# Kernel tuning notes

Measured on AMD Instinct MI355X. Metric: run time of the kernel, lower is better.

The kernel has to match this reference:

```python
import jax, jax.numpy as jnp
import numpy as np

CODEBOOK_SIZE = 1024
EMBED_DIM = 512
DECAY = 0.99
EPS = 1e-05


def setup_inputs() -> dict:
    key = jax.random.key(0)
    k1, k2, k3 = jax.random.split(key, 3)
    z = jax.random.normal(k1, (32, 2048, EMBED_DIM), dtype=jnp.float32)
    embedding = jax.random.normal(k2, (CODEBOOK_SIZE, EMBED_DIM), dtype=jnp.float32)
    cluster_size = jnp.ones((CODEBOOK_SIZE,), dtype=jnp.float32)
    embed_avg = jax.random.normal(k3, (CODEBOOK_SIZE, EMBED_DIM), dtype=jnp.float32)
    return {"z": z, "embedding": embedding, "cluster_size": cluster_size, "embed_avg": embed_avg}


def reference(z, embedding, cluster_size, embed_avg):
    # Flatten tokens: [N, D]
    z_flat = z.reshape(-1, EMBED_DIM)

    # Squared-L2 distances to codebook via expansion: ||z||^2 - 2 z.E^T + ||e||^2 -> [N, K]
    z_sq = jnp.sum(z_flat * z_flat, axis=1, keepdims=True)                 # [N, 1]
    e_sq = jnp.sum(embedding * embedding, axis=1)                          # [K]
    distances = z_sq - 2.0 * (z_flat @ embedding.T) + e_sq[None, :]        # [N, K]
    indices = jnp.argmin(distances, axis=1)                                # [N] int

    # Codebook gather (quantized vectors)
    quantized = embedding[indices].reshape(z.shape)

    # --- EMA codebook update (training-mode math, deterministic part) ---
    used_counts = jax.ops.segment_sum(
        jnp.ones_like(indices, dtype=z_flat.dtype), indices, num_segments=CODEBOOK_SIZE)
    embed_sum = jax.ops.segment_sum(
        jax.lax.stop_gradient(z_flat), indices, num_segments=CODEBOOK_SIZE)  # [K, D]

    new_cluster_size = DECAY * cluster_size + (1.0 - DECAY) * used_counts
    new_embed_avg = DECAY * embed_avg + (1.0 - DECAY) * embed_sum
    n = jnp.sum(new_cluster_size)
    smoothed = (new_cluster_size + EPS) / (n + CODEBOOK_SIZE * EPS) * n
    new_embedding = new_embed_avg / smoothed[:, None]

    # Straight-through estimator
    quantized_st = z + jax.lax.stop_gradient(quantized - z)

    return (quantized_st, indices.reshape(z.shape[:-1]),
            new_embedding, new_cluster_size, new_embed_avg)
```

## Files before the change

### kernel.cpp

```cpp
#include <hip/hip_runtime.h>
#include <cfloat>

#define NTOK 65536
#define DIM  512
#define KCB  1024
#define TAU  0.12f
#define REF_CAP 4096

typedef unsigned short u16;
typedef __attribute__((ext_vector_type(8))) _Float16 half8;
typedef __attribute__((ext_vector_type(4))) float f32x4;

#define AS1(p) ((const __attribute__((address_space(1))) void*)(p))
#define AS3(p) ((__attribute__((address_space(3))) void*)(p))


__device__ __forceinline__ u16 h2u(_Float16 h) {
    u16 u; __builtin_memcpy(&u, &h, 2); return u;
}

__global__ __launch_bounds__(256) void esq_kernel(const float* __restrict__ E,
                                                  float* __restrict__ esq)
{
    const int lane = threadIdx.x & 63;
    const int wv   = threadIdx.x >> 6;
    const int k    = blockIdx.x * 4 + wv;
    const float* er = E + (size_t)k * DIM + lane * 8;
    float4 a = *(const float4*)er;
    float4 b = *(const float4*)(er + 4);
    float s = a.x*a.x + a.y*a.y + a.z*a.z + a.w*a.w
            + b.x*b.x + b.y*b.y + b.z*b.z + b.w*b.w;
    for (int off = 32; off > 0; off >>= 1) s += __shfl_down(s, off, 64);
    if (lane == 0) esq[k] = s;
}

__global__ __launch_bounds__(256) void ehalf_kernel(const float* __restrict__ E,
                                                    u16* __restrict__ Ehf)
{
    const size_t i = (size_t)blockIdx.x * 256 + threadIdx.x;
    const float2 v = *(const float2*)(E + i * 2);
    const _Float16 h0 = (_Float16)v.x, h1 = (_Float16)v.y;
    ((unsigned int*)Ehf)[i] = ((unsigned int)h2u(h1) << 16) | h2u(h0);
}

#define CVT(ZH, ZL, J, VAL) { const _Float16 hv_ = (_Float16)(VAL); \
    (ZH)[J] = hv_; (ZL)[J] = (_Float16)((VAL) - (float)hv_); }

#define LOADK(KC, ZH, ZL) { \
    const float4 a_ = *(const float4*)(zr + (KC) * 32); \
    const float4 b_ = *(const float4*)(zr + (KC) * 32 + 4); \
    CVT(ZH, ZL, 0, a_.x) CVT(ZH, ZL, 1, a_.y) \
    CVT(ZH, ZL, 2, a_.z) CVT(ZH, ZL, 3, a_.w) \
    CVT(ZH, ZL, 4, b_.x) CVT(ZH, ZL, 5, b_.y) \
    CVT(ZH, ZL, 6, b_.z) CVT(ZH, ZL, 7, b_.w) }

#define DSOFF(KC) const int off##KC = lo16 * 512 + \
    (((((KC) << 2) | hi16) ^ lo16) << 3);

#define KSTEP(KC, ZH, ZL) { \
    const half8 eh_ = *(const half8*)&ehi_t[off##KC]; \
    accA = __builtin_amdgcn_mfma_f32_16x16x32_f16((ZH), eh_, accA, 0, 0, 0); \
    accB = __builtin_amdgcn_mfma_f32_16x16x32_f16((ZL), eh_, accB, 0, 0, 0); }

#define STAGE { \
    __builtin_amdgcn_global_load_lds(AS1(gp0), AS3(&ehi_t[c0 * 512]), 16, 0, 0); \
    __builtin_amdgcn_global_load_lds(AS1(gp1), AS3(&ehi_t[c1 * 512]), 16, 0, 0); \
    __builtin_amdgcn_global_load_lds(AS1(gp2), AS3(&ehi_t[c2 * 512]), 16, 0, 0); \
    __builtin_amdgcn_global_load_lds(AS1(gp3), AS3(&ehi_t[c3 * 512]), 16, 0, 0); \
    gp0 += 8192; gp1 += 8192; gp2 += 8192; gp3 += 8192; }

__global__ __launch_bounds__(256, 1) void score_kernel(
    const float* __restrict__ z,
    const u16* __restrict__ Ehf,
    const float* __restrict__ esq,
    int* __restrict__ idx_ws, float* __restrict__ idx_out,
    int* __restrict__ refCount, int* __restrict__ refList)
{
    __shared__ _Float16 ehi_t[16 * 512];
    __shared__ float esq_lds[KCB];

    const int tid  = threadIdx.x;
    const int lane = tid & 63;
    const int wv   = tid >> 6;
    const int lo16 = lane & 15;
    const int hi16 = lane >> 4;
    const int blk  = blockIdx.x;
    const int tokbase = blk * 64 + wv * 16;

    for (int i = tid; i < KCB; i += 256) esq_lds[i] = esq[i];

    const float* zr = z + (size_t)(tokbase + lo16) * DIM + (hi16 << 3);
    half8 zh0,zh1,zh2,zh3,zh4,zh5,zh6,zh7,zh8,zh9,zh10,zh11,zh12,zh13,zh14,zh15;
    half8 zl0,zl1,zl2,zl3,zl4,zl5,zl6,zl7,zl8,zl9,zl10,zl11,zl12,zl13,zl14,zl15;
    LOADK(0,  zh0,  zl0)  LOADK(1,  zh1,  zl1)  LOADK(2,  zh2,  zl2)
    LOADK(3,  zh3,  zl3)  LOADK(4,  zh4,  zl4)  LOADK(5,  zh5,  zl5)
    LOADK(6,  zh6,  zl6)  LOADK(7,  zh7,  zl7)  LOADK(8,  zh8,  zl8)
    LOADK(9,  zh9,  zl9)  LOADK(10, zh10, zl10) LOADK(11, zh11, zl11)
    LOADK(12, zh12, zl12) LOADK(13, zh13, zl13) LOADK(14, zh14, zl14)
    LOADK(15, zh15, zl15)

    DSOFF(0)  DSOFF(1)  DSOFF(2)  DSOFF(3)
    DSOFF(4)  DSOFF(5)  DSOFF(6)  DSOFF(7)
    DSOFF(8)  DSOFF(9)  DSOFF(10) DSOFF(11)
    DSOFF(12) DSOFF(13) DSOFF(14) DSOFF(15)

    const int c0 = (wv << 2), c1 = c0 + 1, c2 = c0 + 2, c3 = c0 + 3;
    const u16* gp0 = Ehf + (size_t)c0 * 512 + ((lane ^ c0) << 3);
    const u16* gp1 = Ehf + (size_t)c1 * 512 + ((lane ^ c1) << 3);
    const u16* gp2 = Ehf + (size_t)c2 * 512 + ((lane ^ c2) << 3);
    const u16* gp3 = Ehf + (size_t)c3 * 512 + ((lane ^ c3) << 3);

    float d1[4], d2[4]; int i1[4];
    #pragma unroll
    for (int r = 0; r < 4; ++r) { d1[r] = FLT_MAX; d2[r] = FLT_MAX; i1[r] = KCB; }

    for (int ch = 0; ch < 64; ++ch) {
        __syncthreads();
        STAGE
        __syncthreads();

        const float ej = esq_lds[(ch << 4) + lo16];
        f32x4 accA = {0.f, 0.f, 0.f, 0.f};
        f32x4 accB = {0.f, 0.f, 0.f, 0.f};
        KSTEP(0,  zh0,  zl0)  KSTEP(1,  zh1,  zl1)  KSTEP(2,  zh2,  zl2)
        KSTEP(3,  zh3,  zl3)  KSTEP(4,  zh4,  zl4)  KSTEP(5,  zh5,  zl5)
        KSTEP(6,  zh6,  zl6)  KSTEP(7,  zh7,  zl7)  KSTEP(8,  zh8,  zl8)
        KSTEP(9,  zh9,  zl9)  KSTEP(10, zh10, zl10) KSTEP(11, zh11, zl11)
        KSTEP(12, zh12, zl12) KSTEP(13, zh13, zl13) KSTEP(14, zh14, zl14)
        KSTEP(15, zh15, zl15)

        const int code = (ch << 4) + lo16;
        #pragma unroll
        for (int r = 0; r < 4; ++r) {
            const float dist = fmaf(-2.0f, accB[r], fmaf(-2.0f, accA[r], ej));
            if (dist < d1[r]) { d2[r] = d1[r]; d1[r] = dist; i1[r] = code; }
            else              { d2[r] = fminf(d2[r], dist); }
        }
    }

    #pragma unroll
    for (int off = 1; off < 16; off <<= 1) {
        #pragma unroll
        for (int r = 0; r < 4; ++r) {
            const float od1 = __shfl_xor(d1[r], off, 64);
            const int   oi1 = __shfl_xor(i1[r], off, 64);
            const float od2 = __shfl_xor(d2[r], off, 64);
            float loser;
            if (od1 < d1[r] || (od1 == d1[r] && oi1 < i1[r])) {
                loser = d1[r]; d1[r] = od1; i1[r] = oi1;
            } else {
                loser = od1;
            }
            d2[r] = fminf(fminf(d2[r], od2), loser);
        }
    }
    if (lo16 == 0) {
        #pragma unroll
        for (int r = 0; r < 4; ++r) {
            const int token = tokbase + (hi16 << 2) + r;
            idx_ws[token]  = i1[r];
            idx_out[token] = (float)i1[r];
            if (d2[r] - d1[r] < TAU) {
                int slot = atomicAdd(refCount, 1);
                if (slot < REF_CAP) refList[slot] = token;
            }
        }
    }
}

__global__ __launch_bounds__(256) void refine_kernel(
    const float* __restrict__ z, const float* __restrict__ E,
    const int* __restrict__ refCount, const int* __restrict__ refList,
    int* __restrict__ idx_ws, float* __restrict__ idx_out)
{
    __shared__ double dists[KCB];
    const int tid = threadIdx.x;
    const int grp = tid >> 4;
    const int q   = tid & 15;
    int rc = *refCount; if (rc > REF_CAP) rc = REF_CAP;
    for (int r = blockIdx.x; r < rc; r += gridDim.x) {
        const int token = refList[r];
        double zr[32];
        {
            const float* zp = z + (size_t)token * DIM + q * 32;
            #pragma unroll
            for (int j = 0; j < 8; ++j) {
                const float4 v = *(const float4*)(zp + j * 4);
                zr[j*4+0] = (double)v.x; zr[j*4+1] = (double)v.y;
                zr[j*4+2] = (double)v.z; zr[j*4+3] = (double)v.w;
            }
        }
        for (int c = grp; c < KCB; c += 32) {
            const int c2 = c + 16;
            const float* ep  = E + (size_t)c  * DIM + q * 32;
            const float* ep2 = E + (size_t)c2 * DIM + q * 32;
            double s = 0.0, s2 = 0.0;
            #pragma unroll
            for (int j = 0; j < 8; ++j) {
                const float4 a = *(const float4*)(ep  + j * 4);
                const float4 b = *(const float4*)(ep2 + j * 4);
                double d;
                d = zr[j*4+0] - (double)a.x; s  = fma(d, d, s);
                d = zr[j*4+1] - (double)a.y; s  = fma(d, d, s);
                d = zr[j*4+2] - (double)a.z; s  = fma(d, d, s);
                d = zr[j*4+3] - (double)a.w; s  = fma(d, d, s);
                d = zr[j*4+0] - (double)b.x; s2 = fma(d, d, s2);
                d = zr[j*4+1] - (double)b.y; s2 = fma(d, d, s2);
                d = zr[j*4+2] - (double)b.z; s2 = fma(d, d, s2);
                d = zr[j*4+3] - (double)b.w; s2 = fma(d, d, s2);
            }
            #pragma unroll
            for (int off = 1; off < 16; off <<= 1) {
                s  += __shfl_xor(s,  off, 64);
                s2 += __shfl_xor(s2, off, 64);
            }
            if (q == 0) { dists[c] = s; dists[c2] = s2; }
        }
        __syncthreads();
        if (tid < 64) {
            const int lane = tid;
            double best = dists[lane]; int bi = lane;
            for (int c = lane + 64; c < KCB; c += 64) {
                const double dv = dists[c];
                if (dv < best) { best = dv; bi = c; }
            }
            for (int off = 32; off > 0; off >>= 1) {
                const double ob = __shfl_down(best, off, 64);
                const int    oi = __shfl_down(bi, off, 64);
                if (ob < best || (ob == best && oi < bi)) { best = ob; bi = oi; }
            }
            if (lane == 0) { idx_ws[token] = bi; idx_out[token] = (float)bi; }
        }
        __syncthreads();
    }
}

__global__ __launch_bounds__(256) void hist_kernel(const int* __restrict__ idx,
                                                   int* __restrict__ counts)
{
    __shared__ int h[KCB];
    const int tid = threadIdx.x;
    for (int i = tid; i < KCB; i += 256) h[i] = 0;
    __syncthreads();
    const int b0 = blockIdx.x * 1024;
    #pragma unroll
    for (int j = 0; j < 4; ++j) atomicAdd(&h[idx[b0 + j * 256 + tid]], 1);
    __syncthreads();
    for (int i = tid; i < KCB; i += 256) {
        const int v = h[i];
        if (v) atomicAdd(&counts[i], v);
    }
}

__global__ __launch_bounds__(1024) void scan_kernel(const int* __restrict__ counts,
                                                    int* __restrict__ cursor,
                                                    int* __restrict__ base)
{
    const int tid = threadIdx.x, lane = tid & 63, wv = tid >> 6;
    const int v = counts[tid];
    int s = v;
    #pragma unroll
    for (int off = 1; off < 64; off <<= 1) {
        const int nb = __shfl_up(s, off, 64);
        if (lane >= off) s += nb;
    }
    __shared__ int wsum[16], wbase[16];
    if (lane == 63) wsum[wv] = s;
    __syncthreads();
    if (tid == 0) {
        int r = 0;
        for (int w = 0; w < 16; ++w) { wbase[w] = r; r += wsum[w]; }
    }
    __syncthreads();
    const int excl = wbase[wv] + s - v;
    cursor[tid] = excl;
    base[tid]   = excl;
}

__global__ __launch_bounds__(256) void scatter_kernel(const int* __restrict__ idx,
                                                      int* __restrict__ cursor,
                                                      int* __restrict__ toklist)
{
    const int b0 = blockIdx.x * 1024;
    #pragma unroll
    for (int j = 0; j < 4; ++j) {
        const int t = b0 + j * 256 + threadIdx.x;
        const int k = idx[t];
        const int slot = atomicAdd(&cursor[k], 1);
        toklist[slot] = t;
    }
}

__global__ __launch_bounds__(256) void seg_sum_kernel(
    const float* __restrict__ z, const float* __restrict__ E,
    const int* __restrict__ toklist, const int* __restrict__ idx,
    float* __restrict__ out0, float* __restrict__ esum)
{
    __shared__ int toks[64];
    __shared__ int ks[64];
    const int tid  = threadIdx.x;
    const int seg0 = blockIdx.x * 64;
    if (tid < 64) toks[tid] = toklist[seg0 + tid];
    __syncthreads();
    if (tid < 64) ks[tid] = idx[toks[tid]];
    __syncthreads();

    const int d = tid * 2;
    int curk = ks[0];
    float2 er  = *(const float2*)(E + (size_t)curk * DIM + d);
    float2 acc = {0.f, 0.f};
    float2 v   = *(const float2*)(z + (size_t)toks[0] * DIM + d);
    for (int i = 0; i < 64; ++i) {
        const int t = toks[i];
        float2 vn;
        if (i < 63) vn = *(const float2*)(z + (size_t)toks[i + 1] * DIM + d);
        const int k = ks[i];
        if (k != curk) {
            atomicAdd(&esum[(size_t)curk * DIM + d],     acc.x);
            atomicAdd(&esum[(size_t)curk * DIM + d + 1], acc.y);
            acc.x = 0.f; acc.y = 0.f;
            curk = k;
            er = *(const float2*)(E + (size_t)k * DIM + d);
        }
        *(float2*)(out0 + (size_t)t * DIM + d) = er;
        acc.x += v.x; acc.y += v.y;
        v = vn;
    }
    atomicAdd(&esum[(size_t)curk * DIM + d],     acc.x);
    atomicAdd(&esum[(size_t)curk * DIM + d + 1], acc.y);
}

__global__ __launch_bounds__(1024) void cs_n_kernel(const float* __restrict__ cs,
    const int* __restrict__ counts, float* __restrict__ out3,
    float* __restrict__ n_ws)
{
    const int k = threadIdx.x;
    const float ncs = 0.99f * cs[k] + 0.01f * (float)counts[k];
    out3[k] = ncs;
    float s = ncs;
    for (int off = 32; off > 0; off >>= 1) s += __shfl_down(s, off, 64);
    __shared__ float red[16];
    const int lane = k & 63, wv = k >> 6;
    if (lane == 0) red[wv] = s;
    __syncthreads();
    if (k == 0) {
        float t = 0.f;
        for (int i = 0; i < 16; ++i) t += red[i];
        n_ws[0] = t;
    }
}

__global__ __launch_bounds__(256) void out24_kernel(const float* __restrict__ ea,
    const float* __restrict__ esum, const float* __restrict__ out3,
    const float* __restrict__ n_ws, float* __restrict__ out2,
    float* __restrict__ out4)
{
    const size_t i = (size_t)blockIdx.x * 256 + threadIdx.x;
    const int k = (int)(i >> 9);
    const float n = n_ws[0];
    const float smoothed = (out3[k] + 1e-5f) / (n + 0.01024f) * n;
    const float nea = 0.99f * ea[i] + 0.01f * esum[i];
    out4[i] = nea;
    out2[i] = nea / smoothed;
}

extern "C" void kernel_launch(void* const* d_in, const int* in_sizes, int n_in,
                              void* d_out, int out_size, void* d_ws, size_t ws_size,
                              hipStream_t stream)
{
    const float* z  = (const float*)d_in[0];
    const float* E  = (const float*)d_in[1];
    const float* cs = (const float*)d_in[2];
    const float* ea = (const float*)d_in[3];

    float* out0 = (float*)d_out;
    float* out1 = out0 + (size_t)NTOK * DIM;
    float* out2 = out1 + NTOK;
    float* out3 = out2 + (size_t)KCB * DIM;
    float* out4 = out3 + KCB;

    char* ws = (char*)d_ws;
    int*   idx_ws  = (int*)ws;
    float* esq     = (float*)(ws + 262144);
    int*   refCnt  = (int*)(ws + 266240);
    int*   refList = (int*)(ws + 266256);
    float* n_ws    = (float*)(ws + 282640);
    int*   counts  = (int*)(ws + 282656);
    int*   cursor  = (int*)(ws + 286752);
    int*   base    = (int*)(ws + 290848);
    u16*   Ehf     = (u16*)(ws + 294976);
    float* esum    = (float*)(ws + 294976);
    int*   toklist = (int*)out2;

    hipMemsetAsync(refCnt, 0, sizeof(int), stream);
    hipMemsetAsync(counts, 0, KCB * sizeof(int), stream);

    esq_kernel<<<KCB / 4, 256, 0, stream>>>(E, esq);
    ehalf_kernel<<<(KCB * DIM / 2) / 256, 256, 0, stream>>>(E, Ehf);
    score_kernel<<<NTOK / 64, 256, 0, stream>>>(z, Ehf, esq, idx_ws, out1, refCnt, refList);
    hipMemsetAsync(esum, 0, (size_t)KCB * DIM * sizeof(float), stream);
    refine_kernel<<<1024, 256, 0, stream>>>(z, E, refCnt, refList, idx_ws, out1);
    hist_kernel<<<NTOK / 1024, 256, 0, stream>>>(idx_ws, counts);
    scan_kernel<<<1, 1024, 0, stream>>>(counts, cursor, base);
    scatter_kernel<<<NTOK / 1024, 256, 0, stream>>>(idx_ws, cursor, toklist);
    seg_sum_kernel<<<NTOK / 64, 256, 0, stream>>>(z, E, toklist, idx_ws, out0, esum);
    cs_n_kernel<<<1, 1024, 0, stream>>>(cs, counts, out3, n_ws);
    out24_kernel<<<(KCB * DIM) / 256, 256, 0, stream>>>(ea, esum, out3, n_ws, out2, out4);
}
```

Measured before the change: 378.8 us.

## Double score block to 8 waves and stage 32 codes per barrier pair

The score kernel now launches 512-thread blocks covering 128 tokens. Each iteration stages 32 codebook rows into a doubled LDS buffer instead of 16, then runs two compute passes per staged chunk. This halves the number of barrier pairs per block and shares each staged codebook tile across twice as many waves. Each block needs more LDS, and with launch bounds (512,2) the register budget may tighten for the large z register tiles, which could cause spills.

```diff
diff --git a/kernel.cpp b/kernel.cpp
--- a/kernel.cpp
+++ b/kernel.cpp
@@ -57,8 +57,8 @@
 #define DSOFF(KC) const int off##KC = lo16 * 512 + \
     (((((KC) << 2) | hi16) ^ lo16) << 3);
 
-#define KSTEP(KC, ZH, ZL) { \
-    const half8 eh_ = *(const half8*)&ehi_t[off##KC]; \
+#define KSTEP(KC, ZH, ZL, HOFF) { \
+    const half8 eh_ = *(const half8*)&ehi_t[off##KC + (HOFF)]; \
     accA = __builtin_amdgcn_mfma_f32_16x16x32_f16((ZH), eh_, accA, 0, 0, 0); \
     accB = __builtin_amdgcn_mfma_f32_16x16x32_f16((ZL), eh_, accB, 0, 0, 0); }
 
@@ -67,16 +67,36 @@
     __builtin_amdgcn_global_load_lds(AS1(gp1), AS3(&ehi_t[c1 * 512]), 16, 0, 0); \
     __builtin_amdgcn_global_load_lds(AS1(gp2), AS3(&ehi_t[c2 * 512]), 16, 0, 0); \
     __builtin_amdgcn_global_load_lds(AS1(gp3), AS3(&ehi_t[c3 * 512]), 16, 0, 0); \
-    gp0 += 8192; gp1 += 8192; gp2 += 8192; gp3 += 8192; }
-
-__global__ __launch_bounds__(256, 1) void score_kernel(
+    gp0 += 16384; gp1 += 16384; gp2 += 16384; gp3 += 16384; }
+
+#define COMPUTE(HOFF, CODE0) { \
+    const int code_ = (CODE0) + lo16; \
+    const float ej = esq_lds[code_]; \
+    f32x4 accA = {0.f, 0.f, 0.f, 0.f}; \
+    f32x4 accB = {0.f, 0.f, 0.f, 0.f}; \
+    KSTEP(0,  zh0,  zl0,  HOFF) KSTEP(1,  zh1,  zl1,  HOFF) \
+    KSTEP(2,  zh2,  zl2,  HOFF) KSTEP(3,  zh3,  zl3,  HOFF) \
+    KSTEP(4,  zh4,  zl4,  HOFF) KSTEP(5,  zh5,  zl5,  HOFF) \
+    KSTEP(6,  zh6,  zl6,  HOFF) KSTEP(7,  zh7,  zl7,  HOFF) \
+    KSTEP(8,  zh8,  zl8,  HOFF) KSTEP(9,  zh9,  zl9,  HOFF) \
+    KSTEP(10, zh10, zl10, HOFF) KSTEP(11, zh11, zl11, HOFF) \
+    KSTEP(12, zh12, zl12, HOFF) KSTEP(13, zh13, zl13, HOFF) \
+    KSTEP(14, zh14, zl14, HOFF) KSTEP(15, zh15, zl15, HOFF) \
+    _Pragma("unroll") \
+    for (int r = 0; r < 4; ++r) { \
+        const float dist = fmaf(-2.0f, accB[r], fmaf(-2.0f, accA[r], ej)); \
+        if (dist < d1[r]) { d2[r] = d1[r]; d1[r] = dist; i1[r] = code_; } \
+        else              { d2[r] = fminf(d2[r], dist); } \
+    } }
+
+__global__ __launch_bounds__(512, 2) void score_kernel(
     const float* __restrict__ z,
     const u16* __restrict__ Ehf,
     const float* __restrict__ esq,
     int* __restrict__ idx_ws, float* __restrict__ idx_out,
     int* __restrict__ refCount, int* __restrict__ refList)
 {
-    __shared__ _Float16 ehi_t[16 * 512];
+    __shared__ _Float16 ehi_t[32 * 512];
     __shared__ float esq_lds[KCB];
 
     const int tid  = threadIdx.x;
@@ -85,9 +105,9 @@
     const int lo16 = lane & 15;
     const int hi16 = lane >> 4;
     const int blk  = blockIdx.x;
-    const int tokbase = blk * 64 + wv * 16;
-
-    for (int i = tid; i < KCB; i += 256) esq_lds[i] = esq[i];
+    const int tokbase = blk * 128 + wv * 16;
+
+    for (int i = tid; i < KCB; i += 512) esq_lds[i] = esq[i];
 
     const float* zr = z + (size_t)(tokbase + lo16) * DIM + (hi16 << 3);
     half8 zh0,zh1,zh2,zh3,zh4,zh5,zh6,zh7,zh8,zh9,zh10,zh11,zh12,zh13,zh14,zh15;
@@ -105,37 +125,21 @@
     DSOFF(12) DSOFF(13) DSOFF(14) DSOFF(15)
 
     const int c0 = (wv << 2), c1 = c0 + 1, c2 = c0 + 2, c3 = c0 + 3;
-    const u16* gp0 = Ehf + (size_t)c0 * 512 + ((lane ^ c0) << 3);
-    const u16* gp1 = Ehf + (size_t)c1 * 512 + ((lane ^ c1) << 3);
-    const u16* gp2 = Ehf + (size_t)c2 * 512 + ((lane ^ c2) << 3);
-    const u16* gp3 = Ehf + (size_t)c3 * 512 + ((lane ^ c3) << 3);
+    const u16* gp0 = Ehf + (size_t)c0 * 512 + ((lane ^ (c0 & 15)) << 3);
+    const u16* gp1 = Ehf + (size_t)c1 * 512 + ((lane ^ (c1 & 15)) << 3);
+    const u16* gp2 = Ehf + (size_t)c2 * 512 + ((lane ^ (c2 & 15)) << 3);
+    const u16* gp3 = Ehf + (size_t)c3 * 512 + ((lane ^ (c3 & 15)) << 3);
 
     float d1[4], d2[4]; int i1[4];
     #pragma unroll
     for (int r = 0; r < 4; ++r) { d1[r] = FLT_MAX; d2[r] = FLT_MAX; i1[r] = KCB; }
 
-    for (int ch = 0; ch < 64; ++ch) {
+    for (int ch = 0; ch < 32; ++ch) {
         __syncthreads();
         STAGE
         __syncthreads();
-
-        const float ej = esq_lds[(ch << 4) + lo16];
-        f32x4 accA = {0.f, 0.f, 0.f, 0.f};
-        f32x4 accB = {0.f, 0.f, 0.f, 0.f};
-        KSTEP(0,  zh0,  zl0)  KSTEP(1,  zh1,  zl1)  KSTEP(2,  zh2,  zl2)
-        KSTEP(3,  zh3,  zl3)  KSTEP(4,  zh4,  zl4)  KSTEP(5,  zh5,  zl5)
-        KSTEP(6,  zh6,  zl6)  KSTEP(7,  zh7,  zl7)  KSTEP(8,  zh8,  zl8)
-        KSTEP(9,  zh9,  zl9)  KSTEP(10, zh10, zl10) KSTEP(11, zh11, zl11)
-        KSTEP(12, zh12, zl12) KSTEP(13, zh13, zl13) KSTEP(14, zh14, zl14)
-        KSTEP(15, zh15, zl15)
-
-        const int code = (ch << 4) + lo16;
-        #pragma unroll
-        for (int r = 0; r < 4; ++r) {
-            const float dist = fmaf(-2.0f, accB[r], fmaf(-2.0f, accA[r], ej));
-            if (dist < d1[r]) { d2[r] = d1[r]; d1[r] = dist; i1[r] = code; }
-            else              { d2[r] = fminf(d2[r], dist); }
-        }
+        COMPUTE(0,    (ch << 5))
+        COMPUTE(8192, (ch << 5) + 16)
     }
 
     #pragma unroll
@@ -397,7 +401,7 @@
 
     esq_kernel<<<KCB / 4, 256, 0, stream>>>(E, esq);
     ehalf_kernel<<<(KCB * DIM / 2) / 256, 256, 0, stream>>>(E, Ehf);
-    score_kernel<<<NTOK / 64, 256, 0, stream>>>(z, Ehf, esq, idx_ws, out1, refCnt, refList);
+    score_kernel<<<NTOK / 128, 512, 0, stream>>>(z, Ehf, esq, idx_ws, out1, refCnt, refList);
     hipMemsetAsync(esum, 0, (size_t)KCB * DIM * sizeof(float), stream);
     refine_kernel<<<1024, 256, 0, stream>>>(z, E, refCnt, refList, idx_ws, out1);
     hist_kernel<<<NTOK / 1024, 256, 0, stream>>>(idx_ws, counts);
```

Measured after the change: 372.6 us. About the same (-1.6%).
